# Kernel tuning notes

Hardware: AMD Instinct MI355X
Metric: run time of the kernel (lower is better)

## Reference

```python
import jax, jax.numpy as jnp
import numpy as np

B, T, D, N = 2, 2048, 1024, 16
DT_RANK = 64  # ceil(D / 16)


def setup_inputs() -> dict:
    key = jax.random.key(0)
    ks = jax.random.split(key, 8)
    x = jax.random.normal(ks[0], (B, T, D), dtype=jnp.float32)
    # Linear weights stored as (out, in) like torch; applied as x @ W.T
    W_B = jax.random.normal(ks[1], (N, D), dtype=jnp.float32) / np.sqrt(D)
    W_C = jax.random.normal(ks[2], (N, D), dtype=jnp.float32) / np.sqrt(D)
    W_dt1 = jax.random.normal(ks[3], (DT_RANK, D), dtype=jnp.float32) / np.sqrt(D)
    W_dt2 = jax.random.normal(ks[4], (D, DT_RANK), dtype=jnp.float32) / np.sqrt(DT_RANK)
    # dt bias init: inverse-softplus of dt sampled log-uniform in [dt_min, dt_max]
    dt_min, dt_max = 1e-3, 1e-1
    u = jax.random.uniform(ks[5], (D,), dtype=jnp.float32)
    dt_init = jnp.clip(jnp.exp(u * (np.log(dt_max) - np.log(dt_min)) + np.log(dt_min)), 1e-4, None)
    b_dt2 = dt_init + jnp.log(-jnp.expm1(-dt_init))
    # log_A: per original non-HiPPO path, A in (0.5, 1.0), broadcast to (D, N)
    a = jax.random.uniform(ks[6], (N,), dtype=jnp.float32) * 0.5 + 0.5
    log_A = jnp.broadcast_to(jnp.log(a)[None, :], (D, N)).copy()
    D_skip = jnp.ones((D,), dtype=jnp.float32)
    return {"x": x, "W_B": W_B, "W_C": W_C, "W_dt1": W_dt1,
            "W_dt2": W_dt2, "b_dt2": b_dt2, "log_A": log_A, "D_skip": D_skip}


def _selective_scan(A_bar, B_bar, C):
    # A_bar, B_bar: (B, T, D, N); C: (B, T, N) -> y: (B, T, D)
    def step(h, inputs):
        a_t, b_t, c_t = inputs  # (B,D,N), (B,D,N), (B,N)
        h = a_t * h + b_t
        y_t = jnp.einsum('bdn,bn->bd', h, c_t)
        return h, y_t

    h0 = jnp.zeros(A_bar.shape[:1] + A_bar.shape[2:], dtype=A_bar.dtype)  # (B,D,N)
    xs = (jnp.moveaxis(A_bar, 1, 0), jnp.moveaxis(B_bar, 1, 0), jnp.moveaxis(C, 1, 0))
    _, ys = jax.lax.scan(step, h0, xs)  # ys: (T, B, D)
    return jnp.moveaxis(ys, 0, 1)


def reference(x, W_B, W_C, W_dt1, W_dt2, b_dt2, log_A, D_skip):
    # Projections
    B_t = jnp.einsum('btd,nd->btn', x, W_B)          # (B,T,N)
    C_t = jnp.einsum('btd,nd->btn', x, W_C)          # (B,T,N)
    dt_raw = jnp.einsum('btr,dr->btd', jnp.einsum('btd,rd->btr', x, W_dt1), W_dt2) + b_dt2
    dt = jax.nn.softplus(dt_raw)                     # (B,T,D)
    A = -jnp.exp(log_A)                              # (D,N), negative
    # Discretization
    A_bar = jnp.exp(dt[..., None] * A[None, None])   # (B,T,D,N)
    dB = (A_bar - 1.0) / (A[None, None] + 1e-8)
    B_bar = dB * x[..., None] * B_t[:, :, None, :]   # (B,T,D,N)
    y = _selective_scan(A_bar, B_bar, C_t)           # (B,T,D)
    return y + D_skip * x
```

## Files before the change

### kernel.cpp

```cpp
#include <hip/hip_runtime.h>
#include <hip/hip_bf16.h>

#define BB 2
#define TT 2048
#define DD 1024
#define NN 16
#define RR 64
#define MM (BB*TT)
#define KDIM DD
#define CHUNK 64
#define NCHUNK (TT/CHUNK)
#define KSPLIT 8

#define DT_OFF 0
#define P_OFF  4194304
#define S_OFF  5242880
#define PP_OFF 6291456

#define LOG2E 1.4426950408889634f

#if __has_builtin(__builtin_amdgcn_exp2f)
#define EXP2(x) __builtin_amdgcn_exp2f(x)
#else
#define EXP2(x) exp2f(x)
#endif

__device__ __forceinline__ float softplus_f(float z) {
    return fmaxf(z, 0.0f) + log1pf(expf(-fabsf(z)));
}

__global__ __launch_bounds__(256) void k_proj96(
    const float* __restrict__ x, const float* __restrict__ W_B,
    const float* __restrict__ W_C, const float* __restrict__ W_dt1,
    float* __restrict__ Pp)
{
    __shared__ float xs[16][68];
    __shared__ float wsT[16][97];

    const int tid = threadIdx.x;
    const int r0 = blockIdx.x * 64;
    const int kbase = blockIdx.y * (KDIM / KSPLIT);
    const int tx = tid & 15;
    const int ty = tid >> 4;

    float acc[4][6];
    #pragma unroll
    for (int i = 0; i < 4; i++)
        #pragma unroll
        for (int j = 0; j < 6; j++) acc[i][j] = 0.0f;

    for (int kc = 0; kc < KDIM / KSPLIT; kc += 16) {
        {
            const int row = tid >> 2;
            const int kq = (tid & 3) * 4;
            float4 v = *(const float4*)(x + (size_t)(r0 + row) * KDIM + kbase + kc + kq);
            xs[kq + 0][row] = v.x; xs[kq + 1][row] = v.y;
            xs[kq + 2][row] = v.z; xs[kq + 3][row] = v.w;
        }
        #pragma unroll
        for (int i = 0; i < 6; i++) {
            const int idx = i * 256 + tid;
            const int c = idx >> 4;
            const int kk = idx & 15;
            const float* wrow; int cc;
            if (c < 16)      { wrow = W_B;   cc = c; }
            else if (c < 32) { wrow = W_C;   cc = c - 16; }
            else             { wrow = W_dt1; cc = c - 32; }
            wsT[kk][c] = wrow[(size_t)cc * KDIM + kbase + kc + kk];
        }
        __syncthreads();
        #pragma unroll
        for (int kk = 0; kk < 16; kk++) {
            const float a0 = xs[kk][ty * 4 + 0];
            const float a1 = xs[kk][ty * 4 + 1];
            const float a2 = xs[kk][ty * 4 + 2];
            const float a3 = xs[kk][ty * 4 + 3];
            #pragma unroll
            for (int j = 0; j < 6; j++) {
                const float b = wsT[kk][tx + j * 16];
                acc[0][j] = fmaf(a0, b, acc[0][j]);
                acc[1][j] = fmaf(a1, b, acc[1][j]);
                acc[2][j] = fmaf(a2, b, acc[2][j]);
                acc[3][j] = fmaf(a3, b, acc[3][j]);
            }
        }
        __syncthreads();
    }

    float* out = Pp + (size_t)blockIdx.y * (MM * 96);
    #pragma unroll
    for (int i = 0; i < 4; i++) {
        const int r = r0 + ty * 4 + i;
        #pragma unroll
        for (int j = 0; j < 6; j++)
            out[(size_t)r * 96 + tx + j * 16] = acc[i][j];
    }
}

__global__ __launch_bounds__(256) void k_dtproj(
    const float* __restrict__ Pp, const float* __restrict__ W_dt2,
    const float* __restrict__ b_dt2, float* __restrict__ dt)
{
    __shared__ float r1s[64][68];
    __shared__ float wsT[64][128];

    const int tid = threadIdx.x;
    const int r0 = blockIdx.x * 64;
    const int d0 = blockIdx.y * 128;

    #pragma unroll
    for (int i = 0; i < 4; i++) {
        const int f = tid + i * 256;
        const int row = f >> 4;
        const int kq = (f & 15) * 4;
        const float* src = Pp + (size_t)(r0 + row) * 96 + 32 + kq;
        float4 s = *(const float4*)(src);
        #pragma unroll
        for (int p = 1; p < KSPLIT; p++) {
            const float4 v = *(const float4*)(src + (size_t)p * MM * 96);
            s.x += v.x; s.y += v.y; s.z += v.z; s.w += v.w;
        }
        *(float4*)&r1s[row][kq] = s;
    }
    {
        const int dl = tid >> 1;
        const int khalf = (tid & 1) * 32;
        const float* src = W_dt2 + (size_t)(d0 + dl) * RR + khalf;
        #pragma unroll
        for (int kq = 0; kq < 32; kq += 4) {
            const float4 v = *(const float4*)(src + kq);
            wsT[khalf + kq + 0][dl] = v.x;
            wsT[khalf + kq + 1][dl] = v.y;
            wsT[khalf + kq + 2][dl] = v.z;
            wsT[khalf + kq + 3][dl] = v.w;
        }
    }
    __syncthreads();

    const int cg = tid & 15;
    const int rg = tid >> 4;

    float4 acc[4][2];
    #pragma unroll
    for (int i = 0; i < 4; i++) {
        acc[i][0] = make_float4(0.f, 0.f, 0.f, 0.f);
        acc[i][1] = make_float4(0.f, 0.f, 0.f, 0.f);
    }

    for (int k4 = 0; k4 < 16; k4++) {
        float r1a[4][4];
        #pragma unroll
        for (int i = 0; i < 4; i++) {
            const float4 v = *(const float4*)&r1s[rg * 4 + i][k4 * 4];
            r1a[i][0] = v.x; r1a[i][1] = v.y; r1a[i][2] = v.z; r1a[i][3] = v.w;
        }
        #pragma unroll
        for (int kk = 0; kk < 4; kk++) {
            const int k = k4 * 4 + kk;
            const float4 w0 = *(const float4*)&wsT[k][cg * 4];
            const float4 w1 = *(const float4*)&wsT[k][64 + cg * 4];
            #pragma unroll
            for (int i = 0; i < 4; i++) {
                const float a = r1a[i][kk];
                acc[i][0].x = fmaf(a, w0.x, acc[i][0].x);
                acc[i][0].y = fmaf(a, w0.y, acc[i][0].y);
                acc[i][0].z = fmaf(a, w0.z, acc[i][0].z);
                acc[i][0].w = fmaf(a, w0.w, acc[i][0].w);
                acc[i][1].x = fmaf(a, w1.x, acc[i][1].x);
                acc[i][1].y = fmaf(a, w1.y, acc[i][1].y);
                acc[i][1].z = fmaf(a, w1.z, acc[i][1].z);
                acc[i][1].w = fmaf(a, w1.w, acc[i][1].w);
            }
        }
    }

    #pragma unroll
    for (int q = 0; q < 2; q++) {
        const float4 bias = *(const float4*)(b_dt2 + d0 + q * 64 + cg * 4);
        #pragma unroll
        for (int i = 0; i < 4; i++) {
            const int row = r0 + rg * 4 + i;
            float4 o;
            o.x = softplus_f(acc[i][q].x + bias.x);
            o.y = softplus_f(acc[i][q].y + bias.y);
            o.z = softplus_f(acc[i][q].z + bias.z);
            o.w = softplus_f(acc[i][q].w + bias.w);
            *(float4*)(dt + (size_t)row * DD + d0 + q * 64 + cg * 4) = o;
        }
    }
}

__global__ __launch_bounds__(256) void k_scan1(
    const float* __restrict__ x, const float* __restrict__ dt,
    const float* __restrict__ Pp, const float* __restrict__ log_A,
    float* __restrict__ P, float* __restrict__ S)
{
    __shared__ float dt_s[CHUNK][64];
    __shared__ float x_s[CHUNK][64];
    __shared__ float bt_s[CHUNK][NN];

    const int tid = threadIdx.x;
    const int ng = tid & 3;
    const int dl = tid >> 2;
    const int d0 = blockIdx.x * 64;
    const int d  = d0 + dl;
    const int c  = blockIdx.y;
    const int b  = blockIdx.z;
    const int n0 = ng * 4;
    const int base = b * TT + c * CHUNK;

    {
        const float* gdt = dt + (size_t)base * DD + d0;
        const float* gx  = x  + (size_t)base * DD + d0;
        #pragma unroll
        for (int k = 0; k < 4; k++) {
            const int f = tid + k * 256;
            const int t = f >> 4;
            const int j = (f & 15) * 4;
            *(float4*)&dt_s[t][j] = *(const float4*)(gdt + (size_t)t * DD + j);
            *(float4*)&x_s[t][j]  = *(const float4*)(gx  + (size_t)t * DD + j);
        }
        const int t = tid >> 2;
        const int jc = (tid & 3) * 4;
        const float* src = Pp + (size_t)(base + t) * 96 + jc;
        float4 s = *(const float4*)(src);
        #pragma unroll
        for (int p = 1; p < KSPLIT; p++) {
            const float4 v = *(const float4*)(src + (size_t)p * MM * 96);
            s.x += v.x; s.y += v.y; s.z += v.z; s.w += v.w;
        }
        const float4 lgj = *(const float4*)(log_A + jc);
        s.x *= 1.0f / (-__expf(lgj.x) + 1e-8f);
        s.y *= 1.0f / (-__expf(lgj.y) + 1e-8f);
        s.z *= 1.0f / (-__expf(lgj.z) + 1e-8f);
        s.w *= 1.0f / (-__expf(lgj.w) + 1e-8f);
        *(float4*)&bt_s[t][jc] = s;
    }

    const float4 lg = *(const float4*)(log_A + d * NN + n0);
    const float A20 = -__expf(lg.x) * LOG2E, A21 = -__expf(lg.y) * LOG2E,
                A22 = -__expf(lg.z) * LOG2E, A23 = -__expf(lg.w) * LOG2E;

    __syncthreads();

    float S0 = 0.f, S1 = 0.f, S2 = 0.f, S3 = 0.f;
    float dtsum = 0.f;

    #pragma unroll 16
    for (int t = 0; t < CHUNK; t++) {
        const float dtv = dt_s[t][dl];
        const float xv  = x_s[t][dl];
        const float4 bt4 = *(const float4*)&bt_s[t][n0];
        const float a0 = EXP2(dtv * A20);
        const float a1 = EXP2(dtv * A21);
        const float a2 = EXP2(dtv * A22);
        const float a3 = EXP2(dtv * A23);
        const float u0 = xv * bt4.x;
        const float u1 = xv * bt4.y;
        const float u2 = xv * bt4.z;
        const float u3 = xv * bt4.w;
        S0 = fmaf(a0, S0 + u0, -u0);
        S1 = fmaf(a1, S1 + u1, -u1);
        S2 = fmaf(a2, S2 + u2, -u2);
        S3 = fmaf(a3, S3 + u3, -u3);
        dtsum += dtv;
    }

    const int oidx = ((c * BB + b) * DD + d) * NN + n0;
    *(float4*)(P + oidx) = make_float4(EXP2(A20 * dtsum), EXP2(A21 * dtsum),
                                       EXP2(A22 * dtsum), EXP2(A23 * dtsum));
    *(float4*)(S + oidx) = make_float4(S0, S1, S2, S3);
}

__global__ __launch_bounds__(256) void k_scan2(
    const float* __restrict__ x, const float* __restrict__ dt,
    const float* __restrict__ Pp, const float* __restrict__ log_A,
    const float* __restrict__ D_skip,
    const float* __restrict__ P, const float* __restrict__ S,
    float* __restrict__ y)
{
    __shared__ float dt_s[CHUNK][64];
    __shared__ float x_s[CHUNK][64];
    __shared__ float bt_s[CHUNK][NN];
    __shared__ float ct_s[CHUNK][NN];

    const int tid = threadIdx.x;
    const int ng = tid & 3;
    const int dl = tid >> 2;
    const int d0 = blockIdx.x * 64;
    const int d  = d0 + dl;
    const int c  = blockIdx.y;
    const int b  = blockIdx.z;
    const int n0 = ng * 4;
    const int base = b * TT + c * CHUNK;

    {
        const float* gdt = dt + (size_t)base * DD + d0;
        const float* gx  = x  + (size_t)base * DD + d0;
        #pragma unroll
        for (int k = 0; k < 4; k++) {
            const int f = tid + k * 256;
            const int t = f >> 4;
            const int j = (f & 15) * 4;
            *(float4*)&dt_s[t][j] = *(const float4*)(gdt + (size_t)t * DD + j);
            *(float4*)&x_s[t][j]  = *(const float4*)(gx  + (size_t)t * DD + j);
        }
        const int t = tid >> 2;
        const int jc = (tid & 3) * 4;
        const float* srcb = Pp + (size_t)(base + t) * 96 + jc;
        const float* srcc = srcb + 16;
        float4 sb = *(const float4*)(srcb);
        float4 sc = *(const float4*)(srcc);
        #pragma unroll
        for (int p = 1; p < KSPLIT; p++) {
            const float4 vb = *(const float4*)(srcb + (size_t)p * MM * 96);
            const float4 vc = *(const float4*)(srcc + (size_t)p * MM * 96);
            sb.x += vb.x; sb.y += vb.y; sb.z += vb.z; sb.w += vb.w;
            sc.x += vc.x; sc.y += vc.y; sc.z += vc.z; sc.w += vc.w;
        }
        const float4 lgj = *(const float4*)(log_A + jc);
        sb.x *= 1.0f / (-__expf(lgj.x) + 1e-8f);
        sb.y *= 1.0f / (-__expf(lgj.y) + 1e-8f);
        sb.z *= 1.0f / (-__expf(lgj.z) + 1e-8f);
        sb.w *= 1.0f / (-__expf(lgj.w) + 1e-8f);
        *(float4*)&bt_s[t][jc] = sb;
        *(float4*)&ct_s[t][jc] = sc;
    }

    const float4 lg = *(const float4*)(log_A + d * NN + n0);
    const float A20 = -__expf(lg.x) * LOG2E, A21 = -__expf(lg.y) * LOG2E,
                A22 = -__expf(lg.z) * LOG2E, A23 = -__expf(lg.w) * LOG2E;
    const float dsk = D_skip[d];

    float h0 = 0.f, h1 = 0.f, h2 = 0.f, h3 = 0.f;
    for (int cc = 0; cc < c; cc++) {
        const int idx = ((cc * BB + b) * DD + d) * NN + n0;
        const float4 Pv = *(const float4*)(P + idx);
        const float4 Sv = *(const float4*)(S + idx);
        h0 = fmaf(Pv.x, h0, Sv.x);
        h1 = fmaf(Pv.y, h1, Sv.y);
        h2 = fmaf(Pv.z, h2, Sv.z);
        h3 = fmaf(Pv.w, h3, Sv.w);
    }
    __syncthreads();

    float* yp = y + (size_t)base * DD + d;

    #pragma unroll 16
    for (int t = 0; t < CHUNK; t++) {
        const float dtv = dt_s[t][dl];
        const float xv  = x_s[t][dl];
        const float4 bt4 = *(const float4*)&bt_s[t][n0];
        const float4 ct4 = *(const float4*)&ct_s[t][n0];
        const float a0 = EXP2(dtv * A20);
        const float a1 = EXP2(dtv * A21);
        const float a2 = EXP2(dtv * A22);
        const float a3 = EXP2(dtv * A23);
        const float u0 = xv * bt4.x;
        const float u1 = xv * bt4.y;
        const float u2 = xv * bt4.z;
        const float u3 = xv * bt4.w;
        h0 = fmaf(a0, h0 + u0, -u0);
        h1 = fmaf(a1, h1 + u1, -u1);
        h2 = fmaf(a2, h2 + u2, -u2);
        h3 = fmaf(a3, h3 + u3, -u3);
        float part = fmaf(h3, ct4.w, fmaf(h2, ct4.z, fmaf(h1, ct4.y, h0 * ct4.x)));
        part += __shfl_xor(part, 1);
        part += __shfl_xor(part, 2);
        if (ng == 0) yp[(size_t)t * DD] = fmaf(dsk, xv, part);
    }
}

extern "C" void kernel_launch(void* const* d_in, const int* in_sizes, int n_in,
                              void* d_out, int out_size, void* d_ws, size_t ws_size,
                              hipStream_t stream)
{
    const float* x      = (const float*)d_in[0];
    const float* W_B    = (const float*)d_in[1];
    const float* W_C    = (const float*)d_in[2];
    const float* W_dt1  = (const float*)d_in[3];
    const float* W_dt2  = (const float*)d_in[4];
    const float* b_dt2  = (const float*)d_in[5];
    const float* log_A  = (const float*)d_in[6];
    const float* D_skip = (const float*)d_in[7];
    float* y = (float*)d_out;

    float* ws = (float*)d_ws;
    float* dt = ws + DT_OFF;
    float* P  = ws + P_OFF;
    float* S  = ws + S_OFF;
    float* Pp = ws + PP_OFF;

    k_proj96<<<dim3(MM / 64, KSPLIT), 256, 0, stream>>>(x, W_B, W_C, W_dt1, Pp);
    k_dtproj<<<dim3(MM / 64, DD / 128), 256, 0, stream>>>(Pp, W_dt2, b_dt2, dt);
    k_scan1<<<dim3(DD / 64, NCHUNK, BB), 256, 0, stream>>>(x, dt, Pp, log_A, P, S);
    k_scan2<<<dim3(DD / 64, NCHUNK, BB), 256, 0, stream>>>(x, dt, Pp, log_A, D_skip, P, S, y);
}
```

Measured before the change: 169.9 us.

## Fuse dt projection and both scan passes into one kernel with grid barrier

Replaces the dt-projection kernel and the two chunked-scan kernels with one fused kernel. Each block computes its dt tile in shared memory from the reduced low-rank projection, runs the chunk summary pass, syncs all blocks through a global atomic barrier, then runs the output pass. A small reduce kernel first collapses the split-K partials into compact B, C and R1 buffers. The aim is to stop writing the full dt tensor to global memory, avoid re-reading dt and x, and remove repeated partial-sum reductions and launches. The software grid barrier only works if all 1024 blocks are resident at once; otherwise it can deadlock.

```diff
diff --git a/kernel.cpp b/kernel.cpp
--- a/kernel.cpp
+++ b/kernel.cpp
@@ -11,11 +11,15 @@
 #define CHUNK 64
 #define NCHUNK (TT/CHUNK)
 #define KSPLIT 8
-
-#define DT_OFF 0
-#define P_OFF  4194304
-#define S_OFF  5242880
-#define PP_OFF 6291456
+#define NBLK ((DD/64)*NCHUNK*BB)
+
+#define BT_OFF 0
+#define CT_OFF 65536
+#define R1_OFF 131072
+#define P_OFF  393216
+#define S_OFF  1441792
+#define PP_OFF 2490368
+#define BAR_OFF 5636096
 
 #define LOG2E 1.4426950408889634f
 
@@ -97,155 +101,184 @@
     }
 }
 
-__global__ __launch_bounds__(256) void k_dtproj(
-    const float* __restrict__ Pp, const float* __restrict__ W_dt2,
-    const float* __restrict__ b_dt2, float* __restrict__ dt)
+__global__ __launch_bounds__(256) void k_reduce96(
+    const float* __restrict__ Pp, const float* __restrict__ log_A,
+    float* __restrict__ Bt, float* __restrict__ Ct, float* __restrict__ R1)
 {
-    __shared__ float r1s[64][68];
-    __shared__ float wsT[64][128];
-
-    const int tid = threadIdx.x;
-    const int r0 = blockIdx.x * 64;
-    const int d0 = blockIdx.y * 128;
-
-    #pragma unroll
-    for (int i = 0; i < 4; i++) {
-        const int f = tid + i * 256;
-        const int row = f >> 4;
-        const int kq = (f & 15) * 4;
-        const float* src = Pp + (size_t)(r0 + row) * 96 + 32 + kq;
-        float4 s = *(const float4*)(src);
-        #pragma unroll
-        for (int p = 1; p < KSPLIT; p++) {
-            const float4 v = *(const float4*)(src + (size_t)p * MM * 96);
-            s.x += v.x; s.y += v.y; s.z += v.z; s.w += v.w;
-        }
-        *(float4*)&r1s[row][kq] = s;
-    }
-    {
-        const int dl = tid >> 1;
-        const int khalf = (tid & 1) * 32;
-        const float* src = W_dt2 + (size_t)(d0 + dl) * RR + khalf;
-        #pragma unroll
-        for (int kq = 0; kq < 32; kq += 4) {
-            const float4 v = *(const float4*)(src + kq);
-            wsT[khalf + kq + 0][dl] = v.x;
-            wsT[khalf + kq + 1][dl] = v.y;
-            wsT[khalf + kq + 2][dl] = v.z;
-            wsT[khalf + kq + 3][dl] = v.w;
-        }
-    }
-    __syncthreads();
-
-    const int cg = tid & 15;
-    const int rg = tid >> 4;
-
-    float4 acc[4][2];
-    #pragma unroll
-    for (int i = 0; i < 4; i++) {
-        acc[i][0] = make_float4(0.f, 0.f, 0.f, 0.f);
-        acc[i][1] = make_float4(0.f, 0.f, 0.f, 0.f);
-    }
-
-    for (int k4 = 0; k4 < 16; k4++) {
-        float r1a[4][4];
-        #pragma unroll
-        for (int i = 0; i < 4; i++) {
-            const float4 v = *(const float4*)&r1s[rg * 4 + i][k4 * 4];
-            r1a[i][0] = v.x; r1a[i][1] = v.y; r1a[i][2] = v.z; r1a[i][3] = v.w;
-        }
-        #pragma unroll
-        for (int kk = 0; kk < 4; kk++) {
-            const int k = k4 * 4 + kk;
-            const float4 w0 = *(const float4*)&wsT[k][cg * 4];
-            const float4 w1 = *(const float4*)&wsT[k][64 + cg * 4];
-            #pragma unroll
-            for (int i = 0; i < 4; i++) {
-                const float a = r1a[i][kk];
-                acc[i][0].x = fmaf(a, w0.x, acc[i][0].x);
-                acc[i][0].y = fmaf(a, w0.y, acc[i][0].y);
-                acc[i][0].z = fmaf(a, w0.z, acc[i][0].z);
-                acc[i][0].w = fmaf(a, w0.w, acc[i][0].w);
-                acc[i][1].x = fmaf(a, w1.x, acc[i][1].x);
-                acc[i][1].y = fmaf(a, w1.y, acc[i][1].y);
-                acc[i][1].z = fmaf(a, w1.z, acc[i][1].z);
-                acc[i][1].w = fmaf(a, w1.w, acc[i][1].w);
-            }
-        }
-    }
-
-    #pragma unroll
-    for (int q = 0; q < 2; q++) {
-        const float4 bias = *(const float4*)(b_dt2 + d0 + q * 64 + cg * 4);
-        #pragma unroll
-        for (int i = 0; i < 4; i++) {
-            const int row = r0 + rg * 4 + i;
-            float4 o;
-            o.x = softplus_f(acc[i][q].x + bias.x);
-            o.y = softplus_f(acc[i][q].y + bias.y);
-            o.z = softplus_f(acc[i][q].z + bias.z);
-            o.w = softplus_f(acc[i][q].w + bias.w);
-            *(float4*)(dt + (size_t)row * DD + d0 + q * 64 + cg * 4) = o;
-        }
-    }
-}
-
-__global__ __launch_bounds__(256) void k_scan1(
-    const float* __restrict__ x, const float* __restrict__ dt,
-    const float* __restrict__ Pp, const float* __restrict__ log_A,
-    float* __restrict__ P, float* __restrict__ S)
-{
-    __shared__ float dt_s[CHUNK][64];
-    __shared__ float x_s[CHUNK][64];
-    __shared__ float bt_s[CHUNK][NN];
-
-    const int tid = threadIdx.x;
-    const int ng = tid & 3;
-    const int dl = tid >> 2;
-    const int d0 = blockIdx.x * 64;
-    const int d  = d0 + dl;
-    const int c  = blockIdx.y;
-    const int b  = blockIdx.z;
-    const int n0 = ng * 4;
-    const int base = b * TT + c * CHUNK;
-
-    {
-        const float* gdt = dt + (size_t)base * DD + d0;
-        const float* gx  = x  + (size_t)base * DD + d0;
-        #pragma unroll
-        for (int k = 0; k < 4; k++) {
-            const int f = tid + k * 256;
-            const int t = f >> 4;
-            const int j = (f & 15) * 4;
-            *(float4*)&dt_s[t][j] = *(const float4*)(gdt + (size_t)t * DD + j);
-            *(float4*)&x_s[t][j]  = *(const float4*)(gx  + (size_t)t * DD + j);
-        }
-        const int t = tid >> 2;
-        const int jc = (tid & 3) * 4;
-        const float* src = Pp + (size_t)(base + t) * 96 + jc;
-        float4 s = *(const float4*)(src);
-        #pragma unroll
-        for (int p = 1; p < KSPLIT; p++) {
-            const float4 v = *(const float4*)(src + (size_t)p * MM * 96);
-            s.x += v.x; s.y += v.y; s.z += v.z; s.w += v.w;
-        }
-        const float4 lgj = *(const float4*)(log_A + jc);
+    const int gid = blockIdx.x * 256 + threadIdx.x;
+    const int e0 = gid * 4;
+    float4 s = *(const float4*)(Pp + e0);
+    #pragma unroll
+    for (int p = 1; p < KSPLIT; p++) {
+        const float4 v = *(const float4*)(Pp + (size_t)p * MM * 96 + e0);
+        s.x += v.x; s.y += v.y; s.z += v.z; s.w += v.w;
+    }
+    const int r = e0 / 96;
+    const int c = e0 - r * 96;
+    if (c < 16) {
+        const float4 lgj = *(const float4*)(log_A + c);
         s.x *= 1.0f / (-__expf(lgj.x) + 1e-8f);
         s.y *= 1.0f / (-__expf(lgj.y) + 1e-8f);
         s.z *= 1.0f / (-__expf(lgj.z) + 1e-8f);
         s.w *= 1.0f / (-__expf(lgj.w) + 1e-8f);
-        *(float4*)&bt_s[t][jc] = s;
-    }
-
+        *(float4*)(Bt + (size_t)r * NN + c) = s;
+    } else if (c < 32) {
+        *(float4*)(Ct + (size_t)r * NN + (c - 16)) = s;
+    } else {
+        *(float4*)(R1 + (size_t)r * RR + (c - 32)) = s;
+    }
+}
+
+__global__ __launch_bounds__(256, 4) void k_fused(
+    const float* __restrict__ x, const float* __restrict__ R1,
+    const float* __restrict__ Bt, const float* __restrict__ Ct,
+    const float* __restrict__ W_dt2, const float* __restrict__ b_dt2,
+    const float* __restrict__ log_A, const float* __restrict__ D_skip,
+    float* __restrict__ P, float* __restrict__ S,
+    float* __restrict__ y, int* bar)
+{
+    __shared__ float dt_s[CHUNK][64];
+    __shared__ float pool[6144];
+    float (*r1s)[64]  = (float (*)[64])pool;
+    float (*wh)[64]   = (float (*)[64])(pool + 4096);
+    float (*x_s)[64]  = (float (*)[64])pool;
+    float (*bt_s)[NN] = (float (*)[NN])(pool + 4096);
+    float (*ct_s)[NN] = (float (*)[NN])(pool + 5120);
+
+    const int tid = threadIdx.x;
+    const int d0 = blockIdx.x * 64;
+    const int c  = blockIdx.y;
+    const int b  = blockIdx.z;
+    const int base = b * TT + c * CHUNK;
+
+    #pragma unroll
+    for (int i = 0; i < 4; i++) {
+        const int f = tid + i * 256;
+        const int row = f >> 4;
+        const int kq = (f & 15) * 4;
+        *(float4*)&r1s[row][kq] = *(const float4*)(R1 + (size_t)(base + row) * RR + kq);
+    }
+    float4 gw0[2], gw1[2];
+    #pragma unroll
+    for (int i = 0; i < 2; i++) {
+        const int f = tid + i * 256;
+        const int dl = f >> 3;
+        const int kq = (f & 7) * 4;
+        gw0[i] = *(const float4*)(W_dt2 + (size_t)(d0 + dl) * RR + kq);
+        gw1[i] = *(const float4*)(W_dt2 + (size_t)(d0 + dl) * RR + 32 + kq);
+    }
+    float4 gx[4];
+    #pragma unroll
+    for (int i = 0; i < 4; i++) {
+        const int f = tid + i * 256;
+        const int t = f >> 4;
+        const int j = (f & 15) * 4;
+        gx[i] = *(const float4*)(x + (size_t)(base + t) * DD + d0 + j);
+    }
+    const int tb = tid >> 2;
+    const int jb = (tid & 3) * 4;
+    const float4 gbt = *(const float4*)(Bt + (size_t)(base + tb) * NN + jb);
+    const float4 gct = *(const float4*)(Ct + (size_t)(base + tb) * NN + jb);
+
+    #pragma unroll
+    for (int i = 0; i < 2; i++) {
+        const int f = tid + i * 256;
+        const int dl = f >> 3;
+        const int kq = (f & 7) * 4;
+        wh[kq + 0][dl] = gw0[i].x; wh[kq + 1][dl] = gw0[i].y;
+        wh[kq + 2][dl] = gw0[i].z; wh[kq + 3][dl] = gw0[i].w;
+    }
+    __syncthreads();
+
+    const int cg = tid & 15;
+    const int rg = tid >> 4;
+    float4 acc4[4];
+    #pragma unroll
+    for (int i = 0; i < 4; i++) acc4[i] = make_float4(0.f, 0.f, 0.f, 0.f);
+
+    #pragma unroll
+    for (int k4 = 0; k4 < 8; k4++) {
+        float4 aa[4];
+        #pragma unroll
+        for (int i = 0; i < 4; i++)
+            aa[i] = *(const float4*)&r1s[rg * 4 + i][k4 * 4];
+        #pragma unroll
+        for (int kk = 0; kk < 4; kk++) {
+            const float4 wv = *(const float4*)&wh[k4 * 4 + kk][cg * 4];
+            #pragma unroll
+            for (int i = 0; i < 4; i++) {
+                const float a = ((const float*)&aa[i])[kk];
+                acc4[i].x = fmaf(a, wv.x, acc4[i].x);
+                acc4[i].y = fmaf(a, wv.y, acc4[i].y);
+                acc4[i].z = fmaf(a, wv.z, acc4[i].z);
+                acc4[i].w = fmaf(a, wv.w, acc4[i].w);
+            }
+        }
+    }
+    __syncthreads();
+    #pragma unroll
+    for (int i = 0; i < 2; i++) {
+        const int f = tid + i * 256;
+        const int dl = f >> 3;
+        const int kq = (f & 7) * 4;
+        wh[kq + 0][dl] = gw1[i].x; wh[kq + 1][dl] = gw1[i].y;
+        wh[kq + 2][dl] = gw1[i].z; wh[kq + 3][dl] = gw1[i].w;
+    }
+    __syncthreads();
+    #pragma unroll
+    for (int k4 = 0; k4 < 8; k4++) {
+        float4 aa[4];
+        #pragma unroll
+        for (int i = 0; i < 4; i++)
+            aa[i] = *(const float4*)&r1s[rg * 4 + i][32 + k4 * 4];
+        #pragma unroll
+        for (int kk = 0; kk < 4; kk++) {
+            const float4 wv = *(const float4*)&wh[k4 * 4 + kk][cg * 4];
+            #pragma unroll
+            for (int i = 0; i < 4; i++) {
+                const float a = ((const float*)&aa[i])[kk];
+                acc4[i].x = fmaf(a, wv.x, acc4[i].x);
+                acc4[i].y = fmaf(a, wv.y, acc4[i].y);
+                acc4[i].z = fmaf(a, wv.z, acc4[i].z);
+                acc4[i].w = fmaf(a, wv.w, acc4[i].w);
+            }
+        }
+    }
+    __syncthreads();
+
+    {
+        const float4 bias = *(const float4*)(b_dt2 + d0 + cg * 4);
+        #pragma unroll
+        for (int i = 0; i < 4; i++) {
+            float4 o;
+            o.x = softplus_f(acc4[i].x + bias.x);
+            o.y = softplus_f(acc4[i].y + bias.y);
+            o.z = softplus_f(acc4[i].z + bias.z);
+            o.w = softplus_f(acc4[i].w + bias.w);
+            *(float4*)&dt_s[rg * 4 + i][cg * 4] = o;
+        }
+    }
+    #pragma unroll
+    for (int i = 0; i < 4; i++) {
+        const int f = tid + i * 256;
+        const int t = f >> 4;
+        const int j = (f & 15) * 4;
+        *(float4*)&x_s[t][j] = gx[i];
+    }
+    *(float4*)&bt_s[tb][jb] = gbt;
+    *(float4*)&ct_s[tb][jb] = gct;
+    __syncthreads();
+
+    const int ng = tid & 3;
+    const int dl = tid >> 2;
+    const int d  = d0 + dl;
+    const int n0 = ng * 4;
     const float4 lg = *(const float4*)(log_A + d * NN + n0);
     const float A20 = -__expf(lg.x) * LOG2E, A21 = -__expf(lg.y) * LOG2E,
                 A22 = -__expf(lg.z) * LOG2E, A23 = -__expf(lg.w) * LOG2E;
-
-    __syncthreads();
-
-    float S0 = 0.f, S1 = 0.f, S2 = 0.f, S3 = 0.f;
-    float dtsum = 0.f;
-
+    const float dsk = D_skip[d];
+
+    float S0 = 0.f, S1 = 0.f, S2 = 0.f, S3 = 0.f, dtsum = 0.f;
     #pragma unroll 16
     for (int t = 0; t < CHUNK; t++) {
         const float dtv = dt_s[t][dl];
@@ -265,72 +298,18 @@
         S3 = fmaf(a3, S3 + u3, -u3);
         dtsum += dtv;
     }
-
     const int oidx = ((c * BB + b) * DD + d) * NN + n0;
     *(float4*)(P + oidx) = make_float4(EXP2(A20 * dtsum), EXP2(A21 * dtsum),
                                        EXP2(A22 * dtsum), EXP2(A23 * dtsum));
     *(float4*)(S + oidx) = make_float4(S0, S1, S2, S3);
-}
-
-__global__ __launch_bounds__(256) void k_scan2(
-    const float* __restrict__ x, const float* __restrict__ dt,
-    const float* __restrict__ Pp, const float* __restrict__ log_A,
-    const float* __restrict__ D_skip,
-    const float* __restrict__ P, const float* __restrict__ S,
-    float* __restrict__ y)
-{
-    __shared__ float dt_s[CHUNK][64];
-    __shared__ float x_s[CHUNK][64];
-    __shared__ float bt_s[CHUNK][NN];
-    __shared__ float ct_s[CHUNK][NN];
-
-    const int tid = threadIdx.x;
-    const int ng = tid & 3;
-    const int dl = tid >> 2;
-    const int d0 = blockIdx.x * 64;
-    const int d  = d0 + dl;
-    const int c  = blockIdx.y;
-    const int b  = blockIdx.z;
-    const int n0 = ng * 4;
-    const int base = b * TT + c * CHUNK;
-
-    {
-        const float* gdt = dt + (size_t)base * DD + d0;
-        const float* gx  = x  + (size_t)base * DD + d0;
-        #pragma unroll
-        for (int k = 0; k < 4; k++) {
-            const int f = tid + k * 256;
-            const int t = f >> 4;
-            const int j = (f & 15) * 4;
-            *(float4*)&dt_s[t][j] = *(const float4*)(gdt + (size_t)t * DD + j);
-            *(float4*)&x_s[t][j]  = *(const float4*)(gx  + (size_t)t * DD + j);
-        }
-        const int t = tid >> 2;
-        const int jc = (tid & 3) * 4;
-        const float* srcb = Pp + (size_t)(base + t) * 96 + jc;
-        const float* srcc = srcb + 16;
-        float4 sb = *(const float4*)(srcb);
-        float4 sc = *(const float4*)(srcc);
-        #pragma unroll
-        for (int p = 1; p < KSPLIT; p++) {
-            const float4 vb = *(const float4*)(srcb + (size_t)p * MM * 96);
-            const float4 vc = *(const float4*)(srcc + (size_t)p * MM * 96);
-            sb.x += vb.x; sb.y += vb.y; sb.z += vb.z; sb.w += vb.w;
-            sc.x += vc.x; sc.y += vc.y; sc.z += vc.z; sc.w += vc.w;
-        }
-        const float4 lgj = *(const float4*)(log_A + jc);
-        sb.x *= 1.0f / (-__expf(lgj.x) + 1e-8f);
-        sb.y *= 1.0f / (-__expf(lgj.y) + 1e-8f);
-        sb.z *= 1.0f / (-__expf(lgj.z) + 1e-8f);
-        sb.w *= 1.0f / (-__expf(lgj.w) + 1e-8f);
-        *(float4*)&bt_s[t][jc] = sb;
-        *(float4*)&ct_s[t][jc] = sc;
-    }
-
-    const float4 lg = *(const float4*)(log_A + d * NN + n0);
-    const float A20 = -__expf(lg.x) * LOG2E, A21 = -__expf(lg.y) * LOG2E,
-                A22 = -__expf(lg.z) * LOG2E, A23 = -__expf(lg.w) * LOG2E;
-    const float dsk = D_skip[d];
+
+    __syncthreads();
+    if (tid == 0) {
+        __hip_atomic_fetch_add(bar, 1, __ATOMIC_ACQ_REL, __HIP_MEMORY_SCOPE_AGENT);
+        while (__hip_atomic_load(bar, __ATOMIC_ACQUIRE, __HIP_MEMORY_SCOPE_AGENT) < NBLK)
+            __builtin_amdgcn_s_sleep(4);
+    }
+    __syncthreads();
 
     float h0 = 0.f, h1 = 0.f, h2 = 0.f, h3 = 0.f;
     for (int cc = 0; cc < c; cc++) {
@@ -342,10 +321,8 @@
         h2 = fmaf(Pv.z, h2, Sv.z);
         h3 = fmaf(Pv.w, h3, Sv.w);
     }
-    __syncthreads();
 
     float* yp = y + (size_t)base * DD + d;
-
     #pragma unroll 16
     for (int t = 0; t < CHUNK; t++) {
         const float dtv = dt_s[t][dl];
@@ -386,13 +363,17 @@
     float* y = (float*)d_out;
 
     float* ws = (float*)d_ws;
-    float* dt = ws + DT_OFF;
+    float* Bt = ws + BT_OFF;
+    float* Ct = ws + CT_OFF;
+    float* R1 = ws + R1_OFF;
     float* P  = ws + P_OFF;
     float* S  = ws + S_OFF;
     float* Pp = ws + PP_OFF;
-
+    int*   bar = (int*)(ws + BAR_OFF);
+
+    hipMemsetAsync(bar, 0, 64, stream);
     k_proj96<<<dim3(MM / 64, KSPLIT), 256, 0, stream>>>(x, W_B, W_C, W_dt1, Pp);
-    k_dtproj<<<dim3(MM / 64, DD / 128), 256, 0, stream>>>(Pp, W_dt2, b_dt2, dt);
-    k_scan1<<<dim3(DD / 64, NCHUNK, BB), 256, 0, stream>>>(x, dt, Pp, log_A, P, S);
-    k_scan2<<<dim3(DD / 64, NCHUNK, BB), 256, 0, stream>>>(x, dt, Pp, log_A, D_skip, P, S, y);
-}
+    k_reduce96<<<dim3(MM * 96 / 4 / 256), 256, 0, stream>>>(Pp, log_A, Bt, Ct, R1);
+    k_fused<<<dim3(DD / 64, NCHUNK, BB), 256, 0, stream>>>(
+        x, R1, Bt, Ct, W_dt2, b_dt2, log_A, D_skip, P, S, y, bar);
+}
```

After: 249.6 us. 1.47x slower.
